# Kernel optimization log

Measured on AMD Instinct MI355X. Metric: run time of the kernel, lower is better.

## Reference

```python
import jax, jax.numpy as jnp
import numpy as np


def _warp2d_transpose(grad_out, u):
    """Adjoint of bilinear warp with zero boundary handling.

    grad_out: [B,H,W,C] incoming gradient (channel-last)
    u:        [B,H,W,2] flow, u[...,0]=dx (horizontal), u[...,1]=dy (vertical)
    Returns grad_x: [B,H,W,C] via flow-guided bilinear scatter-add.
    """
    B, H, W, C = grad_out.shape
    yy, xx = jnp.meshgrid(jnp.arange(H, dtype=grad_out.dtype),
                          jnp.arange(W, dtype=grad_out.dtype), indexing='ij')
    gx = xx[None] + u[..., 0]  # [B,H,W] sample x-coord
    gy = yy[None] + u[..., 1]  # [B,H,W] sample y-coord
    x0f = jnp.floor(gx)
    y0f = jnp.floor(gy)
    wx = gx - x0f  # fractional weights
    wy = gy - y0f
    x0 = x0f.astype(jnp.int32)
    y0 = y0f.astype(jnp.int32)
    x1 = x0 + 1
    y1 = y0 + 1
    bidx = jnp.arange(B, dtype=jnp.int32)[:, None, None]  # broadcast batch index

    grad_x = jnp.zeros((B, H, W, C), dtype=grad_out.dtype)
    corners = (
        (y0, x0, (1.0 - wy) * (1.0 - wx)),
        (y0, x1, (1.0 - wy) * wx),
        (y1, x0, wy * (1.0 - wx)),
        (y1, x1, wy * wx),
    )
    for yi, xi, w in corners:
        valid = (xi >= 0) & (xi < W) & (yi >= 0) & (yi < H)  # mode='zeros'
        w = jnp.where(valid, w, 0.0)
        xi = jnp.clip(xi, 0, W - 1)
        yi = jnp.clip(yi, 0, H - 1)
        grad_x = grad_x.at[bidx, yi, xi].add(w[..., None] * grad_out)
    return grad_x


def setup_inputs() -> dict:
    key = jax.random.key(0)
    k1, k2, k3 = jax.random.split(key, 3)
    B, H, W, C = 8, 512, 512, 16
    grad_out = jax.random.normal(k1, (B, H, W, C), dtype=jnp.float32)
    u = jax.random.normal(k2, (B, H, W, 2), dtype=jnp.float32) * 4.0
    x = jax.random.normal(k3, (B, H, W, C), dtype=jnp.float32)
    return {"grad_out": grad_out, "u": u, "x": x}


def reference(grad_out, u, x):
    # channel_last=True: the TF layer transposes to NCHW, calls the kernel,
    # and transposes back; in jax we keep NHWC throughout (same math).
    # x only determines the output shape/dtype of the adjoint.
    return _warp2d_transpose(grad_out, u)
```

## Files before the change

### kernel.cpp

```cpp
#include <hip/hip_runtime.h>

#define BB 8
#define HH 512
#define WW 512
#define CC 16

__global__ __launch_bounds__(256) void zero_fill_f4(float4* __restrict__ p, int n4)
{
    int i = blockIdx.x * 256 + threadIdx.x;
    if (i < n4) p[i] = make_float4(0.f, 0.f, 0.f, 0.f);
}

__global__ __launch_bounds__(256) void warp_transpose_scatter(
    const float* __restrict__ gout,
    const float* __restrict__ u,
    float* __restrict__ gx)
{
    const int gid = blockIdx.x * 256 + threadIdx.x;
    const int c   = gid & (CC - 1);
    const int p   = gid >> 4;
    const int x   = p & (WW - 1);
    const int y   = (p >> 9) & (HH - 1);
    const int b   = p >> 18;

    const float2 uv = reinterpret_cast<const float2*>(u)[p];
    const float sx = (float)x + uv.x;
    const float sy = (float)y + uv.y;
    const float x0f = floorf(sx);
    const float y0f = floorf(sy);
    const float wx = sx - x0f;
    const float wy = sy - y0f;
    const int x0 = (int)x0f;
    const int y0 = (int)y0f;
    const int x1 = x0 + 1;
    const int y1 = y0 + 1;

    const float g   = gout[gid];
    const float w00 = (1.0f - wy) * (1.0f - wx) * g;
    const float w01 = (1.0f - wy) * wx * g;
    const float w10 = wy * (1.0f - wx) * g;
    const float w11 = wy * wx * g;

    const bool vx0 = (unsigned)x0 < (unsigned)WW;
    const bool vx1 = (unsigned)x1 < (unsigned)WW;
    const bool vy0 = (unsigned)y0 < (unsigned)HH;
    const bool vy1 = (unsigned)y1 < (unsigned)HH;

    const int base = b * (HH * WW);
    if (vy0 && vx0) atomicAdd(&gx[((base + y0 * WW + x0) << 4) + c], w00);
    if (vy0 && vx1) atomicAdd(&gx[((base + y0 * WW + x1) << 4) + c], w01);
    if (vy1 && vx0) atomicAdd(&gx[((base + y1 * WW + x0) << 4) + c], w10);
    if (vy1 && vx1) atomicAdd(&gx[((base + y1 * WW + x1) << 4) + c], w11);
}

extern "C" void kernel_launch(void* const* d_in, const int* in_sizes, int n_in,
                              void* d_out, int out_size, void* d_ws, size_t ws_size,
                              hipStream_t stream) {
    const float* gout = (const float*)d_in[0];
    const float* u    = (const float*)d_in[1];
    float* gx = (float*)d_out;

    const int total = BB * HH * WW * CC;
    const int n4    = total / 4;
    zero_fill_f4<<<(n4 + 255) / 256, 256, 0, stream>>>((float4*)gx, n4);

    const int blocks = total / 256;
    warp_transpose_scatter<<<blocks, 256, 0, stream>>>(gout, u, gx);
}
```

Baseline: 637.7 us.

## Replace global atomic scatter with tiled shared-memory gather plus outlier pass

Each block owns a 16x32 output tile. It scans a halo of source pixels whose flow stays within 15 pixels, compacts the ones that land in the tile, and accumulates their contributions with shared-memory atomics before writing the tile out once. This also removes the separate zero-fill kernel. A second kernel handles large-flow pixels with global atomics after the tile writes. The aim is to cut global atomic traffic and contention, at the cost of rescanning the halo (roughly 6x the tile area of flow reads) and shared-memory atomic conflicts.

```diff
diff --git a/kernel.cpp b/kernel.cpp
--- a/kernel.cpp
+++ b/kernel.cpp
@@ -5,52 +5,146 @@
 #define WW 512
 #define CC 16
 
-__global__ __launch_bounds__(256) void zero_fill_f4(float4* __restrict__ p, int n4)
-{
-    int i = blockIdx.x * 256 + threadIdx.x;
-    if (i < n4) p[i] = make_float4(0.f, 0.f, 0.f, 0.f);
+#define TH 16
+#define TW 32
+#define RR 16
+#define SH (TH + 2*RR)
+#define SW (TW + 2*RR)
+#define NSCAN (SH * SW)
+#define CPAD 17
+
+__device__ __forceinline__ bool flow_small(float ux, float uy) {
+    return (fabsf(ux) <= 15.0f) & (fabsf(uy) <= 15.0f);
 }
 
-__global__ __launch_bounds__(256) void warp_transpose_scatter(
+__global__ __launch_bounds__(256) void warp_t_gather(
     const float* __restrict__ gout,
     const float* __restrict__ u,
     float* __restrict__ gx)
 {
-    const int gid = blockIdx.x * 256 + threadIdx.x;
-    const int c   = gid & (CC - 1);
-    const int p   = gid >> 4;
-    const int x   = p & (WW - 1);
-    const int y   = (p >> 9) & (HH - 1);
-    const int b   = p >> 18;
+    __shared__ float acc[TH * TW * CPAD];
+    __shared__ unsigned short lst[NSCAN];
+    __shared__ int cnt;
 
-    const float2 uv = reinterpret_cast<const float2*>(u)[p];
-    const float sx = (float)x + uv.x;
-    const float sy = (float)y + uv.y;
-    const float x0f = floorf(sx);
-    const float y0f = floorf(sy);
-    const float wx = sx - x0f;
-    const float wy = sy - y0f;
+    const int tid = threadIdx.x;
+    const int bid = blockIdx.x;
+    const int b   = bid >> 9;
+    const int t   = bid & 511;
+    const int ty0 = (t >> 4) * TH;
+    const int tx0 = (t & 15) * TW;
+
+    for (int i = tid; i < TH * TW * CPAD; i += 256) acc[i] = 0.0f;
+    if (tid == 0) cnt = 0;
+    __syncthreads();
+
+    const float2* ub = (const float2*)(u) + (size_t)b * (HH * WW);
+
+    for (int i = tid; i < NSCAN; i += 256) {
+        const int sy = ty0 - RR + (i >> 6);
+        const int sx = tx0 - RR + (i & 63);
+        if ((unsigned)sy >= (unsigned)HH || (unsigned)sx >= (unsigned)WW) continue;
+        const float2 uv = ub[sy * WW + sx];
+        if (!flow_small(uv.x, uv.y)) continue;
+        const float fx = (float)sx + uv.x;
+        const float fy = (float)sy + uv.y;
+        const int lx0 = (int)floorf(fx) - tx0;
+        const int ly0 = (int)floorf(fy) - ty0;
+        if (lx0 >= -1 && lx0 < TW && ly0 >= -1 && ly0 < TH) {
+            const int k = atomicAdd(&cnt, 1);
+            lst[k] = (unsigned short)i;
+        }
+    }
+    __syncthreads();
+    const int n = cnt;
+
+    for (int e = tid; e < n; e += 256) {
+        const int i  = lst[e];
+        const int sy = ty0 - RR + (i >> 6);
+        const int sx = tx0 - RR + (i & 63);
+        const float2 uv = ub[sy * WW + sx];
+        const float fx = (float)sx + uv.x;
+        const float fy = (float)sy + uv.y;
+        const float x0f = floorf(fx);
+        const float y0f = floorf(fy);
+        const float wx = fx - x0f;
+        const float wy = fy - y0f;
+        const int lx0 = (int)x0f - tx0;
+        const int ly0 = (int)y0f - ty0;
+
+        const float4* gp =
+            (const float4*)(gout + ((size_t)((b * HH + sy) * WW + sx) << 4));
+        const float4 g0 = gp[0], g1 = gp[1], g2 = gp[2], g3 = gp[3];
+        float gg[16] = { g0.x, g0.y, g0.z, g0.w,
+                         g1.x, g1.y, g1.z, g1.w,
+                         g2.x, g2.y, g2.z, g2.w,
+                         g3.x, g3.y, g3.z, g3.w };
+        const float w00 = (1.0f - wy) * (1.0f - wx);
+        const float w01 = (1.0f - wy) * wx;
+        const float w10 = wy * (1.0f - wx);
+        const float w11 = wy * wx;
+        const float ws4[4] = { w00, w01, w10, w11 };
+
+#pragma unroll
+        for (int cor = 0; cor < 4; cor++) {
+            const int lx = lx0 + (cor & 1);
+            const int ly = ly0 + (cor >> 1);
+            if ((unsigned)lx < (unsigned)TW && (unsigned)ly < (unsigned)TH) {
+                const float w = ws4[cor];
+                const int base = (ly * TW + lx) * CPAD;
+#pragma unroll
+                for (int j = 0; j < 16; j++)
+                    atomicAdd(&acc[base + j], w * gg[j]);
+            }
+        }
+    }
+    __syncthreads();
+
+    for (int i = tid; i < TH * TW * CC; i += 256) {
+        const int pix = i >> 4;
+        const int c   = i & 15;
+        const int ly  = pix >> 5;
+        const int lx  = pix & 31;
+        gx[((size_t)((b * HH + ty0 + ly) * WW + tx0 + lx) << 4) + c] =
+            acc[pix * CPAD + c];
+    }
+}
+
+__global__ __launch_bounds__(256) void warp_t_outlier(
+    const float* __restrict__ gout,
+    const float* __restrict__ u,
+    float* __restrict__ gx)
+{
+    const int p = blockIdx.x * 256 + threadIdx.x;
+    const float2 uv = ((const float2*)u)[p];
+    if (flow_small(uv.x, uv.y)) return;
+
+    const int x = p & (WW - 1);
+    const int y = (p >> 9) & (HH - 1);
+    const int b = p >> 18;
+    const float fx = (float)x + uv.x;
+    const float fy = (float)y + uv.y;
+    const float x0f = floorf(fx);
+    const float y0f = floorf(fy);
+    const float wx = fx - x0f;
+    const float wy = fy - y0f;
     const int x0 = (int)x0f;
     const int y0 = (int)y0f;
-    const int x1 = x0 + 1;
-    const int y1 = y0 + 1;
 
-    const float g   = gout[gid];
-    const float w00 = (1.0f - wy) * (1.0f - wx) * g;
-    const float w01 = (1.0f - wy) * wx * g;
-    const float w10 = wy * (1.0f - wx) * g;
-    const float w11 = wy * wx * g;
-
-    const bool vx0 = (unsigned)x0 < (unsigned)WW;
-    const bool vx1 = (unsigned)x1 < (unsigned)WW;
-    const bool vy0 = (unsigned)y0 < (unsigned)HH;
-    const bool vy1 = (unsigned)y1 < (unsigned)HH;
-
-    const int base = b * (HH * WW);
-    if (vy0 && vx0) atomicAdd(&gx[((base + y0 * WW + x0) << 4) + c], w00);
-    if (vy0 && vx1) atomicAdd(&gx[((base + y0 * WW + x1) << 4) + c], w01);
-    if (vy1 && vx0) atomicAdd(&gx[((base + y1 * WW + x0) << 4) + c], w10);
-    if (vy1 && vx1) atomicAdd(&gx[((base + y1 * WW + x1) << 4) + c], w11);
+    const float* gp = gout + ((size_t)p << 4);
+    const float ws4[4] = { (1.0f - wy) * (1.0f - wx), (1.0f - wy) * wx,
+                           wy * (1.0f - wx),          wy * wx };
+#pragma unroll
+    for (int cor = 0; cor < 4; cor++) {
+        const int xx = x0 + (cor & 1);
+        const int yy = y0 + (cor >> 1);
+        if ((unsigned)xx < (unsigned)WW && (unsigned)yy < (unsigned)HH) {
+            const float w = ws4[cor];
+            float* dst = gx + ((size_t)((b * HH + yy) * WW + xx) << 4);
+#pragma unroll
+            for (int j = 0; j < 16; j++)
+                atomicAdd(dst + j, w * gp[j]);
+        }
+    }
 }
 
 extern "C" void kernel_launch(void* const* d_in, const int* in_sizes, int n_in,
@@ -60,10 +154,9 @@
     const float* u    = (const float*)d_in[1];
     float* gx = (float*)d_out;
 
-    const int total = BB * HH * WW * CC;
-    const int n4    = total / 4;
-    zero_fill_f4<<<(n4 + 255) / 256, 256, 0, stream>>>((float4*)gx, n4);
+    const int tiles = BB * (HH / TH) * (WW / TW);
+    warp_t_gather<<<tiles, 256, 0, stream>>>(gout, u, gx);
 
-    const int blocks = total / 256;
-    warp_transpose_scatter<<<blocks, 256, 0, stream>>>(gout, u, gx);
+    const int pixels = BB * HH * WW;
+    warp_t_outlier<<<pixels / 256, 256, 0, stream>>>(gout, u, gx);
 }
```

New measurement: 944.7 us. +48.1%, slower.
